# Kernel optimization log

Hardware: AMD Instinct MI355X
Metric: run time of the kernel (lower is better)

The kernel has to match this reference:

```python
import jax, jax.numpy as jnp
import numpy as np

EPS_COS = 1e-8
EPS_SHARP = 1e-16


def setup_inputs() -> dict:
    key = jax.random.key(0)
    k1, k2, k3, k4 = jax.random.split(key, 4)
    B, H, R, C, M = 512, 512, 2048, 64, 3
    out_dim = 3 * C + 2 * M + 4  # 202
    h = jax.random.normal(k1, (B, H), dtype=jnp.float32)
    prev_w = jax.random.uniform(k2, (B, R), dtype=jnp.float32)
    prev_w = prev_w / prev_w.sum(axis=1, keepdims=True)  # valid focus distribution
    memory = jax.random.normal(k3, (B, R, C), dtype=jnp.float32)
    fc_w = jax.random.normal(k4, (out_dim, H), dtype=jnp.float32) * 0.05
    fc_b = jnp.zeros((out_dim,), dtype=jnp.float32)
    return {"h": h, "prev_w": prev_w, "memory": memory, "fc_w": fc_w, "fc_b": fc_b}


def _write_head(h, prev_w, memory, fc_w, fc_b):
    B, R, C = memory.shape
    total = fc_w.shape[0]
    shift_len = total - 3 * C - 3          # 2*max_shift + 1
    m = (shift_len - 1) // 2               # max_shift

    z = h @ fc_w.T + fc_b                  # [B, total]
    sizes = [C, 1, 1, shift_len, 1, C, C]
    offs = np.cumsum([0] + sizes)
    k     = jnp.tanh(z[:, offs[0]:offs[1]])                 # [B, C]
    beta  = jax.nn.softplus(z[:, offs[1]:offs[2]])          # [B, 1]
    g     = jax.nn.sigmoid(z[:, offs[2]:offs[3]])           # [B, 1]
    s     = jax.nn.softmax(z[:, offs[3]:offs[4]], axis=1)   # [B, 2m+1]
    gamma = jax.nn.softplus(z[:, offs[4]:offs[5]]) + 1.0    # [B, 1]
    e     = jax.nn.sigmoid(z[:, offs[5]:offs[6]])           # [B, C]
    a     = jnp.tanh(z[:, offs[6]:offs[7]])                 # [B, C]

    # content addressing: cosine similarity of k vs each memory row
    num = jnp.einsum('bc,brc->br', k, memory)
    k_n = jnp.maximum(jnp.linalg.norm(k, axis=1, keepdims=True), EPS_COS)   # [B,1]
    m_n = jnp.maximum(jnp.linalg.norm(memory, axis=2), EPS_COS)             # [B,R]
    w_c = jax.nn.softmax(beta * (num / (k_n * m_n)), axis=1)                # [B,R]

    # gated interpolation
    w_g = g * w_c + (1.0 - g) * prev_w                                      # [B,R]

    # circular shift (per-sample cross-correlation, O(B*R*(2m+1)))
    unrolled = jnp.concatenate([w_g[:, -m:], w_g, w_g[:, :m]], axis=1)      # [B, R+2m]
    windows = jnp.stack([unrolled[:, j:j + R] for j in range(2 * m + 1)], axis=1)  # [B,2m+1,R]
    w_s = jnp.einsum('bjr,bj->br', windows, s)                              # [B,R]

    # sharpen
    w_p = jnp.power(w_s, gamma)
    w = w_p / (w_p.sum(axis=1, keepdims=True) + EPS_SHARP)                  # [B,R]

    # erase + write (fused)
    wE = w[:, :, None]                                                      # [B,R,1]
    new_mem = memory * (1.0 - wE * e[:, None, :]) + wE * a[:, None, :]      # [B,R,C]
    return w, new_mem


def reference(h, prev_w, memory, fc_w, fc_b):
    return _write_head(h, prev_w, memory, fc_w, fc_b)
```

## Files before the change

kernel.cpp:

```cpp
#include <hip/hip_runtime.h>
#include <math.h>

#define BB 512
#define HH 512
#define RR 2048
#define CC 64
#define OUTD 202
#define PSTRIDE 208
#define K_OFF 0
#define E_OFF 64
#define A_OFF 128
#define S_OFF 192
#define COMBO_OFF 199
#define G_OFF 200
#define GAMMA_OFF 201

typedef float f32x4 __attribute__((ext_vector_type(4)));

__device__ __forceinline__ float softplusf_(float x) {
    return (x > 20.f) ? x : log1pf(expf(x));
}
__device__ __forceinline__ float sigmoidf_(float x) {
    return 1.f / (1.f + expf(-x));
}

__global__ __launch_bounds__(256) void params_kernel(
    const float* __restrict__ h, const float* __restrict__ fc_w,
    const float* __restrict__ fc_b, float* __restrict__ pw)
{
    __shared__ float h_sh[HH];
    __shared__ float z_sh[80];
    const int b = blockIdx.x;
    const int tid = threadIdx.x;
    float* p = pw + (size_t)b * PSTRIDE;

    *(float2*)(h_sh + tid * 2) = *(const float2*)(h + (size_t)b * HH + tid * 2);
    __syncthreads();

    if (tid < OUTD) {
        const float4* wr = (const float4*)(fc_w + (size_t)tid * HH);
        float acc = 0.f;
        #pragma unroll 4
        for (int i = 0; i < HH / 4; ++i) {
            float4 wv = wr[i];
            acc += wv.x * h_sh[4 * i]     + wv.y * h_sh[4 * i + 1]
                 + wv.z * h_sh[4 * i + 2] + wv.w * h_sh[4 * i + 3];
        }
        float z = acc + fc_b[tid];
        if (tid < 74) z_sh[tid] = z;
        if (tid < 64)                      p[K_OFF + tid] = tanhf(z);
        else if (tid == 65)                p[G_OFF] = sigmoidf_(z);
        else if (tid == 73)                p[GAMMA_OFF] = softplusf_(z) + 1.f;
        else if (tid >= 74 && tid < 138)   p[E_OFF + (tid - 74)] = sigmoidf_(z);
        else if (tid >= 138)               p[A_OFF + (tid - 138)] = tanhf(z);
    }
    __syncthreads();

    if (tid < 64) {
        float kv = tanhf(z_sh[tid]);
        float ss = kv * kv;
        #pragma unroll
        for (int m = 1; m < 64; m <<= 1) ss += __shfl_xor(ss, m, 64);
        if (tid == 0) {
            float kn = fmaxf(sqrtf(ss), 1e-8f);
            float beta = softplusf_(z_sh[64]);
            p[COMBO_OFF] = beta / kn;
            float mx = -1e30f;
            #pragma unroll
            for (int q = 0; q < 7; ++q) mx = fmaxf(mx, z_sh[66 + q]);
            float ev[7], se = 0.f;
            #pragma unroll
            for (int q = 0; q < 7; ++q) {
                ev[q] = __expf(z_sh[66 + q] - mx);
                se += ev[q];
            }
            float inv = 1.f / se;
            #pragma unroll
            for (int q = 0; q < 7; ++q) p[S_OFF + q] = ev[q] * inv;
        }
    }
}

__device__ __forceinline__ float block_reduce_sum4(float v, float* red) {
    #pragma unroll
    for (int m = 1; m < 64; m <<= 1) v += __shfl_xor(v, m, 64);
    int wid = threadIdx.x >> 6;
    if ((threadIdx.x & 63) == 0) red[wid] = v;
    __syncthreads();
    float x = red[0] + red[1] + red[2] + red[3];
    __syncthreads();
    return x;
}

__global__ __launch_bounds__(256) void score_kernel(
    const float* __restrict__ memory, const float* __restrict__ pw,
    float* __restrict__ sc, float* __restrict__ esum)
{
    __shared__ float red[4];
    const int tid = threadIdx.x;
    const int b = blockIdx.x >> 2;
    const int rbase = (blockIdx.x & 3) * 512;
    const int lane8 = tid & 7;
    const int rgrp = tid >> 3;
    const float* p = pw + (size_t)b * PSTRIDE;
    const f32x4 ka = *(const f32x4*)(p + K_OFF + lane8 * 8);
    const f32x4 kb = *(const f32x4*)(p + K_OFF + lane8 * 8 + 4);
    const float combo = p[COMBO_OFF];
    const float* memb = memory + (size_t)b * RR * CC;

    float lsum = 0.f;
    #pragma unroll
    for (int mi = 0; mi < 4; ++mi) {
        f32x4 ma[4], mb[4];
        #pragma unroll
        for (int j = 0; j < 4; ++j) {
            int r = rbase + (mi * 4 + j) * 32 + rgrp;
            const f32x4* mp = (const f32x4*)(memb + (size_t)r * CC + lane8 * 8);
            ma[j] = mp[0];
            mb[j] = mp[1];
        }
        #pragma unroll
        for (int j = 0; j < 4; ++j) {
            int r = rbase + (mi * 4 + j) * 32 + rgrp;
            float num = ma[j].x * ka.x + ma[j].y * ka.y + ma[j].z * ka.z
                      + ma[j].w * ka.w + mb[j].x * kb.x + mb[j].y * kb.y
                      + mb[j].z * kb.z + mb[j].w * kb.w;
            float ssq = ma[j].x * ma[j].x + ma[j].y * ma[j].y
                      + ma[j].z * ma[j].z + ma[j].w * ma[j].w
                      + mb[j].x * mb[j].x + mb[j].y * mb[j].y
                      + mb[j].z * mb[j].z + mb[j].w * mb[j].w;
            #pragma unroll
            for (int m = 1; m < 8; m <<= 1) {
                num += __shfl_xor(num, m, 64);
                ssq += __shfl_xor(ssq, m, 64);
            }
            if (lane8 == 0) {
                float mn = fmaxf(sqrtf(ssq), 1e-8f);
                float ev = __expf(combo * num / mn);
                sc[(size_t)b * RR + r] = ev;
                lsum += ev;
            }
        }
    }
    float bs = block_reduce_sum4(lsum, red);
    if (tid == 0) esum[blockIdx.x] = bs;
}

__device__ __forceinline__ float block_reduce_sum16(float v, float* red) {
    #pragma unroll
    for (int m = 1; m < 64; m <<= 1) v += __shfl_xor(v, m, 64);
    int wid = threadIdx.x >> 6;
    if ((threadIdx.x & 63) == 0) red[wid] = v;
    __syncthreads();
    if (threadIdx.x < 16) {
        float x = red[threadIdx.x];
        #pragma unroll
        for (int m = 1; m < 16; m <<= 1) x += __shfl_xor(x, m, 64);
        if (threadIdx.x == 0) red[0] = x;
    }
    __syncthreads();
    float r = red[0];
    __syncthreads();
    return r;
}

__global__ __launch_bounds__(1024) void wu_kernel(
    const float* __restrict__ memory, const float* __restrict__ sc,
    const float* __restrict__ esum, const float* __restrict__ prev_w,
    const float* __restrict__ pw, float* __restrict__ out_w,
    float* __restrict__ out_mem)
{
    __shared__ float wg[RR];
    __shared__ float wps[RR];
    __shared__ float red[16];

    const int b = blockIdx.x;
    const int tid = threadIdx.x;
    const float* p = pw + (size_t)b * PSTRIDE;
    const float g = p[G_OFF];
    const float gamma = p[GAMMA_OFF];
    const float s0 = p[S_OFF + 0], s1 = p[S_OFF + 1], s2 = p[S_OFF + 2],
                s3 = p[S_OFF + 3], s4 = p[S_OFF + 4], s5 = p[S_OFF + 5],
                s6 = p[S_OFF + 6];
    const float* eb = esum + (size_t)b * 4;
    const float se = eb[0] + eb[1] + eb[2] + eb[3];
    const float gi = g / se, omg = 1.f - g;

    {
        const int r2 = tid * 2;
        float2 ev = *(const float2*)(sc + (size_t)b * RR + r2);
        float2 pv = *(const float2*)(prev_w + (size_t)b * RR + r2);
        wg[r2]     = gi * ev.x + omg * pv.x;
        wg[r2 + 1] = gi * ev.y + omg * pv.y;
    }
    __syncthreads();

    float lp = 0.f;
    {
        const int r2 = tid * 2;
        #pragma unroll
        for (int q = 0; q < 2; ++q) {
            int r = r2 + q;
            float acc = s0 * wg[(r - 3) & (RR - 1)]
                      + s1 * wg[(r - 2) & (RR - 1)]
                      + s2 * wg[(r - 1) & (RR - 1)]
                      + s3 * wg[r]
                      + s4 * wg[(r + 1) & (RR - 1)]
                      + s5 * wg[(r + 2) & (RR - 1)]
                      + s6 * wg[(r + 3) & (RR - 1)];
            float v = __powf(acc, gamma);
            wps[r] = v;
            lp += v;
        }
    }
    const float ps = block_reduce_sum16(lp, red);
    const float invp = 1.f / (ps + 1e-16f);

    {
        const int r2 = tid * 2;
        float w0 = wps[r2] * invp;
        float w1 = wps[r2 + 1] * invp;
        wg[r2] = w0;
        wg[r2 + 1] = w1;
        *(float2*)(out_w + (size_t)b * RR + r2) = make_float2(w0, w1);
    }
    __syncthreads();

    const int lane8 = tid & 7;
    const int rgrp = tid >> 3;
    const f32x4 ea = *(const f32x4*)(p + E_OFF + lane8 * 8);
    const f32x4 eb2 = *(const f32x4*)(p + E_OFF + lane8 * 8 + 4);
    const f32x4 aa = *(const f32x4*)(p + A_OFF + lane8 * 8);
    const f32x4 ab = *(const f32x4*)(p + A_OFF + lane8 * 8 + 4);
    const float* memb = memory + (size_t)b * RR * CC;
    float* omb = out_mem + (size_t)b * RR * CC;

    #pragma unroll
    for (int mi = 0; mi < 4; ++mi) {
        f32x4 ma[4], mb[4];
        float wv[4];
        #pragma unroll
        for (int j = 0; j < 4; ++j) {
            int r = (mi * 4 + j) * 128 + rgrp;
            const f32x4* mp = (const f32x4*)(memb + (size_t)r * CC + lane8 * 8);
            ma[j] = mp[0];
            mb[j] = mp[1];
            wv[j] = wg[r];
        }
        #pragma unroll
        for (int j = 0; j < 4; ++j) {
            int r = (mi * 4 + j) * 128 + rgrp;
            f32x4 oa, ob;
            oa.x = ma[j].x * (1.f - wv[j] * ea.x) + wv[j] * aa.x;
            oa.y = ma[j].y * (1.f - wv[j] * ea.y) + wv[j] * aa.y;
            oa.z = ma[j].z * (1.f - wv[j] * ea.z) + wv[j] * aa.z;
            oa.w = ma[j].w * (1.f - wv[j] * ea.w) + wv[j] * aa.w;
            ob.x = mb[j].x * (1.f - wv[j] * eb2.x) + wv[j] * ab.x;
            ob.y = mb[j].y * (1.f - wv[j] * eb2.y) + wv[j] * ab.y;
            ob.z = mb[j].z * (1.f - wv[j] * eb2.z) + wv[j] * ab.z;
            ob.w = mb[j].w * (1.f - wv[j] * eb2.w) + wv[j] * ab.w;
            f32x4* op = (f32x4*)(omb + (size_t)r * CC + lane8 * 8);
            op[0] = oa;
            op[1] = ob;
        }
    }
}

extern "C" void kernel_launch(void* const* d_in, const int* in_sizes, int n_in,
                              void* d_out, int out_size, void* d_ws, size_t ws_size,
                              hipStream_t stream) {
    const float* h      = (const float*)d_in[0];
    const float* prev_w = (const float*)d_in[1];
    const float* memory = (const float*)d_in[2];
    const float* fc_w   = (const float*)d_in[3];
    const float* fc_b   = (const float*)d_in[4];

    float* pw      = (float*)d_ws;
    float* out_w   = (float*)d_out;
    float* out_mem = out_w + (size_t)BB * RR;

    const size_t pw_f   = (size_t)BB * PSTRIDE;
    const size_t br_f   = (size_t)BB * RR;
    const size_t need_f = pw_f + br_f + (size_t)BB * 4;

    params_kernel<<<BB, 256, 0, stream>>>(h, fc_w, fc_b, pw);

    if (ws_size >= need_f * sizeof(float)) {
        float* sc   = pw + pw_f;
        float* esum = sc + br_f;
        score_kernel<<<BB * 4, 256, 0, stream>>>(memory, pw, sc, esum);
        wu_kernel<<<BB, 1024, 0, stream>>>(memory, sc, esum, prev_w, pw,
                                           out_w, out_mem);
    } else {
        float* sc   = out_mem;
        float* esum = pw + pw_f;
        score_kernel<<<BB * 4, 256, 0, stream>>>(memory, pw, sc, esum);
        wu_kernel<<<BB, 1024, 0, stream>>>(memory, sc, esum, prev_w, pw,
                                           out_w, out_mem);
    }
}
```

Baseline: 204.9 us.

## Batch the FC projection over 8 samples with split-K partials; narrow score row groups

The linear layer is split into a partial kernel where each block handles 8 batch rows and a quarter of the hidden dimension. Each fc_w load is reused across 8 samples, and a separate combine kernel sums the partials and applies the activations. This cuts the repeated per-sample reads of fc_w in the old params kernel, at the cost of an extra launch and a partials buffer in workspace. The score kernel also changes from 8 lanes per row with two float4 loads each to 16 lanes per row with one float4, which lowers registers per thread and adds a shuffle stage.

```diff
diff --git a/kernel.cpp b/kernel.cpp
--- a/kernel.cpp
+++ b/kernel.cpp
@@ -15,6 +15,8 @@
 #define G_OFF 200
 #define GAMMA_OFF 201
 
+#define PART_STRIDE 224
+
 typedef float f32x4 __attribute__((ext_vector_type(4)));
 
 __device__ __forceinline__ float softplusf_(float x) {
@@ -24,29 +26,60 @@
     return 1.f / (1.f + expf(-x));
 }
 
-__global__ __launch_bounds__(256) void params_kernel(
+__global__ __launch_bounds__(256) void params_part_kernel(
     const float* __restrict__ h, const float* __restrict__ fc_w,
-    const float* __restrict__ fc_b, float* __restrict__ pw)
+    float* __restrict__ part)
 {
-    __shared__ float h_sh[HH];
+    __shared__ float h_sh[8][128];
+    const int tid = threadIdx.x;
+    const int bg = blockIdx.x >> 2;
+    const int hq = blockIdx.x & 3;
+    const int b0 = bg * 8;
+    const int h0 = hq * 128;
+
+    for (int idx = tid; idx < 8 * 128; idx += 256) {
+        int j = idx >> 7, i = idx & 127;
+        h_sh[j][i] = h[(size_t)(b0 + j) * HH + h0 + i];
+    }
+    __syncthreads();
+
+    if (tid < OUTD) {
+        float acc[8];
+        #pragma unroll
+        for (int j = 0; j < 8; ++j) acc[j] = 0.f;
+        const float4* wr = (const float4*)(fc_w + (size_t)tid * HH + h0);
+        #pragma unroll 4
+        for (int i4 = 0; i4 < 32; ++i4) {
+            float4 wv = wr[i4];
+            int i = i4 * 4;
+            #pragma unroll
+            for (int j = 0; j < 8; ++j) {
+                acc[j] = fmaf(wv.x, h_sh[j][i + 0], acc[j]);
+                acc[j] = fmaf(wv.y, h_sh[j][i + 1], acc[j]);
+                acc[j] = fmaf(wv.z, h_sh[j][i + 2], acc[j]);
+                acc[j] = fmaf(wv.w, h_sh[j][i + 3], acc[j]);
+            }
+        }
+        #pragma unroll
+        for (int j = 0; j < 8; ++j) {
+            part[((size_t)(b0 + j) * 4 + hq) * PART_STRIDE + tid] = acc[j];
+        }
+    }
+}
+
+__global__ __launch_bounds__(256) void params_combine_kernel(
+    const float* __restrict__ part, const float* __restrict__ fc_b,
+    float* __restrict__ pw)
+{
     __shared__ float z_sh[80];
     const int b = blockIdx.x;
     const int tid = threadIdx.x;
     float* p = pw + (size_t)b * PSTRIDE;
 
-    *(float2*)(h_sh + tid * 2) = *(const float2*)(h + (size_t)b * HH + tid * 2);
-    __syncthreads();
-
     if (tid < OUTD) {
-        const float4* wr = (const float4*)(fc_w + (size_t)tid * HH);
-        float acc = 0.f;
-        #pragma unroll 4
-        for (int i = 0; i < HH / 4; ++i) {
-            float4 wv = wr[i];
-            acc += wv.x * h_sh[4 * i]     + wv.y * h_sh[4 * i + 1]
-                 + wv.z * h_sh[4 * i + 2] + wv.w * h_sh[4 * i + 3];
-        }
-        float z = acc + fc_b[tid];
+        const float* q = part + (size_t)b * 4 * PART_STRIDE + tid;
+        float z = q[0] + q[PART_STRIDE] + q[2 * PART_STRIDE]
+                + q[3 * PART_STRIDE] + fc_b[tid];
         if (tid < 74) z_sh[tid] = z;
         if (tid < 64)                      p[K_OFF + tid] = tanhf(z);
         else if (tid == 65)                p[G_OFF] = sigmoidf_(z);
@@ -100,46 +133,30 @@
     const int tid = threadIdx.x;
     const int b = blockIdx.x >> 2;
     const int rbase = (blockIdx.x & 3) * 512;
-    const int lane8 = tid & 7;
-    const int rgrp = tid >> 3;
+    const int lane16 = tid & 15;
+    const int rgrp = tid >> 4;
     const float* p = pw + (size_t)b * PSTRIDE;
-    const f32x4 ka = *(const f32x4*)(p + K_OFF + lane8 * 8);
-    const f32x4 kb = *(const f32x4*)(p + K_OFF + lane8 * 8 + 4);
+    const float4 k4 = *(const float4*)(p + K_OFF + lane16 * 4);
     const float combo = p[COMBO_OFF];
     const float* memb = memory + (size_t)b * RR * CC;
 
     float lsum = 0.f;
-    #pragma unroll
-    for (int mi = 0; mi < 4; ++mi) {
-        f32x4 ma[4], mb[4];
-        #pragma unroll
-        for (int j = 0; j < 4; ++j) {
-            int r = rbase + (mi * 4 + j) * 32 + rgrp;
-            const f32x4* mp = (const f32x4*)(memb + (size_t)r * CC + lane8 * 8);
-            ma[j] = mp[0];
-            mb[j] = mp[1];
-        }
-        #pragma unroll
-        for (int j = 0; j < 4; ++j) {
-            int r = rbase + (mi * 4 + j) * 32 + rgrp;
-            float num = ma[j].x * ka.x + ma[j].y * ka.y + ma[j].z * ka.z
-                      + ma[j].w * ka.w + mb[j].x * kb.x + mb[j].y * kb.y
-                      + mb[j].z * kb.z + mb[j].w * kb.w;
-            float ssq = ma[j].x * ma[j].x + ma[j].y * ma[j].y
-                      + ma[j].z * ma[j].z + ma[j].w * ma[j].w
-                      + mb[j].x * mb[j].x + mb[j].y * mb[j].y
-                      + mb[j].z * mb[j].z + mb[j].w * mb[j].w;
-            #pragma unroll
-            for (int m = 1; m < 8; m <<= 1) {
-                num += __shfl_xor(num, m, 64);
-                ssq += __shfl_xor(ssq, m, 64);
-            }
-            if (lane8 == 0) {
-                float mn = fmaxf(sqrtf(ssq), 1e-8f);
-                float ev = __expf(combo * num / mn);
-                sc[(size_t)b * RR + r] = ev;
-                lsum += ev;
-            }
+    #pragma unroll 8
+    for (int i = 0; i < 32; ++i) {
+        int r = rbase + i * 16 + rgrp;
+        float4 m4 = *(const float4*)(memb + (size_t)r * CC + lane16 * 4);
+        float num = m4.x * k4.x + m4.y * k4.y + m4.z * k4.z + m4.w * k4.w;
+        float ssq = m4.x * m4.x + m4.y * m4.y + m4.z * m4.z + m4.w * m4.w;
+        #pragma unroll
+        for (int m = 1; m < 16; m <<= 1) {
+            num += __shfl_xor(num, m, 64);
+            ssq += __shfl_xor(ssq, m, 64);
+        }
+        if (lane16 == 0) {
+            float mn = fmaxf(sqrtf(ssq), 1e-8f);
+            float ev = __expf(combo * num / mn);
+            sc[(size_t)b * RR + r] = ev;
+            lsum += ev;
         }
     }
     float bs = block_reduce_sum4(lsum, red);
@@ -281,21 +298,28 @@
 
     const size_t pw_f   = (size_t)BB * PSTRIDE;
     const size_t br_f   = (size_t)BB * RR;
-    const size_t need_f = pw_f + br_f + (size_t)BB * 4;
-
-    params_kernel<<<BB, 256, 0, stream>>>(h, fc_w, fc_b, pw);
+    const size_t es_f   = (size_t)BB * 4;
+    const size_t part_f = (size_t)BB * 4 * PART_STRIDE;
+    const size_t need_f = pw_f + br_f + es_f + part_f;
+
+    float* sc   = pw + pw_f;
+    float* esum = sc + br_f;
+    float* part = esum + es_f;
 
     if (ws_size >= need_f * sizeof(float)) {
-        float* sc   = pw + pw_f;
-        float* esum = sc + br_f;
+        params_part_kernel<<<256, 256, 0, stream>>>(h, fc_w, part);
+        params_combine_kernel<<<BB, 256, 0, stream>>>(part, fc_b, pw);
         score_kernel<<<BB * 4, 256, 0, stream>>>(memory, pw, sc, esum);
         wu_kernel<<<BB, 1024, 0, stream>>>(memory, sc, esum, prev_w, pw,
                                            out_w, out_mem);
     } else {
-        float* sc   = out_mem;
-        float* esum = pw + pw_f;
-        score_kernel<<<BB * 4, 256, 0, stream>>>(memory, pw, sc, esum);
-        wu_kernel<<<BB, 1024, 0, stream>>>(memory, sc, esum, prev_w, pw,
+        float* sc_fb   = out_mem;
+        float* esum_fb = pw + pw_f;
+        float* part_fb = esum_fb + es_f;
+        params_part_kernel<<<256, 256, 0, stream>>>(h, fc_w, part_fb);
+        params_combine_kernel<<<BB, 256, 0, stream>>>(part_fb, fc_b, pw);
+        score_kernel<<<BB * 4, 256, 0, stream>>>(memory, pw, sc_fb, esum_fb);
+        wu_kernel<<<BB, 1024, 0, stream>>>(memory, sc_fb, esum_fb, prev_w, pw,
                                            out_w, out_mem);
     }
 }
```

New measurement: 191.4 us. 6.6% less time.
